# Performance work log

Hardware: AMD Instinct MI355X
Metric: run time of the kernel (lower is better)

## Reference

```python
import jax, jax.numpy as jnp
import numpy as np

EPS = 1e-12  # matches torch F.normalize eps

def _l2norm(v, axis):
    n = jnp.linalg.norm(v, axis=axis, keepdims=True)
    return v / jnp.maximum(n, EPS)

def setup_inputs() -> dict:
    key = jax.random.key(0)
    k1, k2 = jax.random.split(key)
    x = jax.random.normal(k1, (16, 512, 64, 64), dtype=jnp.float32)
    mem = jax.random.normal(k2, (1024, 512), dtype=jnp.float32)
    memory = _l2norm(mem, axis=1)  # buffer initialized normalized, as in __init__
    return {"x": x, "memory": memory}

def reference(x, memory):
    B, C, H, W = x.shape
    feat = x.transpose(0, 2, 3, 1).reshape(-1, C)          # [N, C], N=B*H*W
    feat_norm = _l2norm(feat, axis=1)                       # [N, C]
    mem_norm = _l2norm(memory, axis=1)                      # [K, C]
    sim = feat_norm @ mem_norm.T                            # [N, K] cosine sims
    attn = jax.nn.softmax(sim, axis=1)                      # [N, K]
    recon = attn @ mem_norm                                 # [N, C]
    recon = recon.reshape(B, H, W, C).transpose(0, 3, 1, 2) # [B, C, H, W]
    match_map = attn.max(axis=1).reshape(B, H, W)           # [B, H, W]
    return recon, match_map
```

## Files before the change

kernel.cpp:

```cpp
#include <hip/hip_runtime.h>

#define C_DIM 512
#define K_MEM 1024

typedef __attribute__((ext_vector_type(8))) short short8;
typedef __attribute__((ext_vector_type(4))) float f32x4;
typedef __attribute__((ext_vector_type(16))) float f32x16;
typedef __attribute__((ext_vector_type(4))) unsigned int u32x4;

#define LGKM0()  asm volatile("s_waitcnt lgkmcnt(0)" ::: "memory")
#define VM0()    asm volatile("s_waitcnt vmcnt(0)" ::: "memory")
#define BAR()    { asm volatile("" ::: "memory"); __builtin_amdgcn_s_barrier(); asm volatile("" ::: "memory"); }

#define GLOAD16(dst, addr, imm) \
    asm volatile("global_load_dwordx4 %0, %1, off offset:%c2" \
                 : "=v"(dst) : "v"(addr), "n"(imm))
#define WAITV(N) do { asm volatile("s_waitcnt vmcnt(%c0)" :: "n"(N) : "memory"); \
                      __builtin_amdgcn_sched_barrier(0); } while (0)

__device__ __forceinline__ unsigned short f2bf(float f) {
    unsigned int u = __builtin_bit_cast(unsigned int, f);
    unsigned int r = (u + 0x7fffu + ((u >> 16) & 1u)) >> 16;
    return (unsigned short)r;
}

__device__ __forceinline__ f32x4 mfma16(short8 a, short8 b, f32x4 c) {
    return __builtin_amdgcn_mfma_f32_16x16x32_bf16(a, b, c, 0, 0, 0);
}
__device__ __forceinline__ f32x16 mfma32(short8 a, short8 b, f32x16 c) {
    return __builtin_amdgcn_mfma_f32_32x32x16_bf16(a, b, c, 0, 0, 0);
}

__device__ __forceinline__ void gl_lds16(const void* g, void* l) {
    __builtin_amdgcn_global_load_lds(
        (const __attribute__((address_space(1))) unsigned int*)g,
        (__attribute__((address_space(3))) unsigned int*)l, 16, 0, 0);
}

__global__ __launch_bounds__(256)
void prep_norm(const float* __restrict__ mem, unsigned short* __restrict__ Mn) {
    int k = blockIdx.x, t = threadIdx.x;
    const float* row = mem + (size_t)k * C_DIM;
    float2 v = *reinterpret_cast<const float2*>(row + 2 * t);
    float ss = v.x * v.x + v.y * v.y;
#pragma unroll
    for (int off = 32; off >= 1; off >>= 1) ss += __shfl_xor(ss, off);
    __shared__ float wp[4];
    if ((t & 63) == 0) wp[t >> 6] = ss;
    __syncthreads();
    float tot = wp[0] + wp[1] + wp[2] + wp[3];
    float rn = 1.0f / fmaxf(sqrtf(tot), 1e-12f);
    unsigned int pk = (unsigned int)f2bf(v.x * rn) | ((unsigned int)f2bf(v.y * rn) << 16);
    *reinterpret_cast<unsigned int*>(Mn + (size_t)k * C_DIM + 2 * t) = pk;
}

__global__ __launch_bounds__(256)
void prep_transpose(const unsigned short* __restrict__ Mn, unsigned short* __restrict__ MnT) {
    __shared__ unsigned short tl[64][72];
    int t = threadIdx.x;
    int bk = blockIdx.x & 15, bc = blockIdx.x >> 4;
    int k0 = bk * 64, c0 = bc * 64;
    {
        int kr = t >> 2, gc = (t & 3) * 16;
        const u32x4* src = reinterpret_cast<const u32x4*>(Mn + (size_t)(k0 + kr) * C_DIM + c0 + gc);
        u32x4 a = src[0], b = src[1];
        *reinterpret_cast<u32x4*>(&tl[kr][gc]) = a;
        *reinterpret_cast<u32x4*>(&tl[kr][gc + 8]) = b;
    }
    __syncthreads();
    {
        int cr = t >> 2, gk = (t & 3) * 16;
        unsigned int ow[8];
#pragma unroll
        for (int j = 0; j < 8; ++j)
            ow[j] = (unsigned int)tl[gk + 2 * j][cr] | ((unsigned int)tl[gk + 2 * j + 1][cr] << 16);
        unsigned int* dst = reinterpret_cast<unsigned int*>(MnT + (size_t)(c0 + cr) * K_MEM + k0 + gk);
#pragma unroll
        for (int j = 0; j < 8; ++j) dst[j] = ow[j];
    }
}

__global__ __launch_bounds__(512)
void normx_kernel(const float* __restrict__ x, unsigned short* __restrict__ Fn) {
    __shared__ alignas(16) char FnB[65536];
    __shared__ float normpart[64][9];
    __shared__ float rnormS[64];
    const int t = threadIdx.x, bid = blockIdx.x;
    const int b = bid >> 6, h = bid & 63;
    const int lane = t & 63, wv = t >> 6;
    const int w = lane, cg = wv;
    const float* xp = x + (size_t)b * 2097152 + (size_t)(cg * 64) * 4096 + (size_t)h * 64 + w;
    float xv[64];
#pragma unroll
    for (int i = 0; i < 64; ++i) xv[i] = xp[(size_t)i * 4096];
    float ss = 0.f;
#pragma unroll
    for (int i = 0; i < 64; ++i) ss += xv[i] * xv[i];
    normpart[w][cg] = ss;
    __syncthreads();
    if (t < 64) {
        float s = 0.f;
#pragma unroll
        for (int j = 0; j < 8; ++j) s += normpart[t][j];
        rnormS[t] = 1.0f / fmaxf(sqrtf(s), 1e-12f);
    }
    __syncthreads();
    float rn = rnormS[w];
    char* fnrow = FnB + w * 1024;
#pragma unroll
    for (int j = 0; j < 8; ++j) {
        u32x4 pk4;
#pragma unroll
        for (int p = 0; p < 4; ++p) {
            float v0 = xv[j * 8 + 2 * p] * rn;
            float v1 = xv[j * 8 + 2 * p + 1] * rn;
            pk4[p] = (unsigned int)f2bf(v0) | ((unsigned int)f2bf(v1) << 16);
        }
        int gs = (cg * 8 + j) ^ (w & 31);
        *(u32x4*)(fnrow + (gs << 4)) = pk4;
    }
    __syncthreads();
    const int r = t >> 3;
    char* orow = (char*)(Fn + (size_t)(bid * 64 + r) * C_DIM);
#pragma unroll
    for (int p = 0; p < 8; ++p) {
        int gl = p * 8 + (t & 7);
        u32x4 v = *(const u32x4*)(FnB + r * 1024 + ((gl ^ (r & 31)) << 4));
        *(u32x4*)(orow + gl * 16) = v;
    }
}

__device__ __forceinline__ void stage_tile(const char* g0, size_t rowBytes, int col0,
                                           char* lds0, int wv, int lane) {
#pragma unroll
    for (int j = 0; j < 4; ++j) {
        const int chunk = wv * 4 + j;
        const int r = chunk * 8 + (lane >> 3);
        const int gs = (lane & 7) ^ (r & 7);
        const char* src = g0 + (size_t)r * rowBytes + col0 + gs * 16;
        gl_lds16(src, lds0 + chunk * 1024);
    }
}

#define FRAG(base, r, gk) (*(const short8*)((base) + (r) * 128 + ((((gk)) ^ ((r) & 7)) << 4)))

__global__ __launch_bounds__(256, 3)
void gemm1_kernel(const unsigned short* __restrict__ Fn, const unsigned short* __restrict__ Mn,
                  unsigned short* __restrict__ P, float* __restrict__ Zp, float* __restrict__ Mp) {
    __shared__ alignas(16) char LDSU[34816];
    __shared__ float zS[128][2], zM[128][2];
    char* As = LDSU;
    char* Bs = LDSU + 16384;

    const int wg = (blockIdx.x & 7) * 512 + (blockIdx.x >> 3);
    const int mt = wg >> 3, nt = wg & 7;
    const int m0 = mt * 128, n0 = nt * 128;
    const int t = threadIdx.x, lane = t & 63, wv = t >> 6;
    const int wm = wv >> 1, wn = wv & 1;
    const int l15 = lane & 15, l4 = lane >> 4;

    const char* Ag = (const char*)Fn + (size_t)m0 * 1024;
    const char* Bg = (const char*)Mn + (size_t)n0 * 1024;

    f32x4 acc[4][4];
#pragma unroll
    for (int i = 0; i < 4; ++i)
#pragma unroll
        for (int j = 0; j < 4; ++j) acc[i][j] = (f32x4){0.f, 0.f, 0.f, 0.f};

#pragma unroll 1
    for (int kt = 0; kt < 8; ++kt) {
        stage_tile(Ag, 1024, kt * 128, As, wv, lane);
        stage_tile(Bg, 1024, kt * 128, Bs, wv, lane);
        VM0(); BAR();
#pragma unroll
        for (int ks = 0; ks < 2; ++ks) {
            short8 af[4], bfr[4];
#pragma unroll
            for (int i = 0; i < 4; ++i) {
                af[i]  = FRAG(As, wm * 64 + i * 16 + l15, ks * 4 + l4);
                bfr[i] = FRAG(Bs, wn * 64 + i * 16 + l15, ks * 4 + l4);
            }
#pragma unroll
            for (int mf = 0; mf < 4; ++mf)
#pragma unroll
                for (int nf = 0; nf < 4; ++nf)
                    acc[mf][nf] = mfma16(af[mf], bfr[nf], acc[mf][nf]);
        }
        LGKM0(); BAR();
    }

    float zsum[4][4], zmax[4][4];
#pragma unroll
    for (int mf = 0; mf < 4; ++mf)
#pragma unroll
        for (int r = 0; r < 4; ++r) { zsum[mf][r] = 0.f; zmax[mf][r] = 0.f; }
#pragma unroll
    for (int mf = 0; mf < 4; ++mf)
#pragma unroll
        for (int nf = 0; nf < 4; ++nf)
#pragma unroll
            for (int r = 0; r < 4; ++r) {
                float e = __expf(acc[mf][nf][r]);
                acc[mf][nf][r] = e;
                zsum[mf][r] += e;
                zmax[mf][r] = fmaxf(zmax[mf][r], e);
            }
#pragma unroll
    for (int off = 1; off < 16; off <<= 1)
#pragma unroll
        for (int mf = 0; mf < 4; ++mf)
#pragma unroll
            for (int r = 0; r < 4; ++r) {
                zsum[mf][r] += __shfl_xor(zsum[mf][r], off);
                zmax[mf][r] = fmaxf(zmax[mf][r], __shfl_xor(zmax[mf][r], off));
            }
    if (l15 == 0) {
#pragma unroll
        for (int mf = 0; mf < 4; ++mf)
#pragma unroll
            for (int r = 0; r < 4; ++r) {
                int row = wm * 64 + mf * 16 + l4 * 4 + r;
                zS[row][wn] = zsum[mf][r];
                zM[row][wn] = zmax[mf][r];
            }
    }
    char* Pscr = LDSU;
#pragma unroll
    for (int mf = 0; mf < 4; ++mf)
#pragma unroll
        for (int nf = 0; nf < 4; ++nf)
#pragma unroll
            for (int r = 0; r < 4; ++r) {
                int row = wm * 64 + mf * 16 + l4 * 4 + r;
                int col = wn * 64 + nf * 16 + l15;
                *(unsigned short*)(Pscr + row * 272 + col * 2) = f2bf(acc[mf][nf][r]);
            }
    LGKM0(); BAR();
    if (t < 128) {
        float zq = zS[t][0] + zS[t][1];
        float mq = fmaxf(zM[t][0], zM[t][1]);
        Zp[(size_t)(m0 + t) * 8 + nt] = zq;
        Mp[(size_t)(m0 + t) * 8 + nt] = mq;
    }
#pragma unroll
    for (int p = 0; p < 8; ++p) {
        int r = (t >> 4) + p * 16;
        u32x4 v = *(const u32x4*)(Pscr + r * 272 + (t & 15) * 16);
        *(u32x4*)((char*)P + (size_t)(m0 + r) * 2048 + n0 * 2 + (t & 15) * 16) = v;
    }
}

__global__ __launch_bounds__(256)
void stats_kernel(const float* __restrict__ Zp, const float* __restrict__ Mp,
                  float* __restrict__ Zinv, float* __restrict__ match) {
    int i = blockIdx.x * 256 + threadIdx.x;
    f32x4 a = *(const f32x4*)(Zp + (size_t)i * 8);
    f32x4 b = *(const f32x4*)(Zp + (size_t)i * 8 + 4);
    float s = (a[0] + a[1] + a[2] + a[3]) + (b[0] + b[1] + b[2] + b[3]);
    f32x4 c = *(const f32x4*)(Mp + (size_t)i * 8);
    f32x4 d = *(const f32x4*)(Mp + (size_t)i * 8 + 4);
    float m = fmaxf(fmaxf(fmaxf(c[0], c[1]), fmaxf(c[2], c[3])),
                    fmaxf(fmaxf(d[0], d[1]), fmaxf(d[2], d[3])));
    float zi = 1.0f / s;
    Zinv[i] = zi;
    match[i] = m * zi;
}

__global__ __launch_bounds__(256, 3)
void gemm2_kernel(const unsigned short* __restrict__ P, const unsigned short* __restrict__ MnT,
                  const float* __restrict__ Zinv, float* __restrict__ recon) {
    __shared__ alignas(16) char As[16384];
    __shared__ alignas(16) char Bs[16384];
    __shared__ float zinvS[128];

    const int wg = (blockIdx.x & 7) * 256 + (blockIdx.x >> 3);
    const int mt = wg >> 2, nt = wg & 3;
    const int m0 = mt * 128, n0 = nt * 128;
    const int t = threadIdx.x, lane = t & 63, wv = t >> 6;
    const int wm = wv >> 1, wn = wv & 1;
    const int l15 = lane & 15, l4 = lane >> 4;

    if (t < 128) zinvS[t] = Zinv[m0 + t];

    const char* Ag = (const char*)P + (size_t)m0 * 2048;
    const char* Bg = (const char*)MnT + (size_t)n0 * 2048;

    f32x4 acc[4][4];
#pragma unroll
    for (int i = 0; i < 4; ++i)
#pragma unroll
        for (int j = 0; j < 4; ++j) acc[i][j] = (f32x4){0.f, 0.f, 0.f, 0.f};

#pragma unroll 1
    for (int kt = 0; kt < 16; ++kt) {
        stage_tile(Ag, 2048, kt * 128, As, wv, lane);
        stage_tile(Bg, 2048, kt * 128, Bs, wv, lane);
        VM0(); BAR();
#pragma unroll
        for (int ks = 0; ks < 2; ++ks) {
            short8 af[4], bfr[4];
#pragma unroll
            for (int i = 0; i < 4; ++i) {
                af[i]  = FRAG(As, wm * 64 + i * 16 + l15, ks * 4 + l4);
                bfr[i] = FRAG(Bs, wn * 64 + i * 16 + l15, ks * 4 + l4);
            }
#pragma unroll
            for (int mf = 0; mf < 4; ++mf)
#pragma unroll
                for (int nf = 0; nf < 4; ++nf)
                    acc[mf][nf] = mfma16(af[mf], bfr[nf], acc[mf][nf]);
        }
        LGKM0(); BAR();
    }

    const int b = m0 >> 12;
    const int inb0 = m0 & 4095;
#pragma unroll
    for (int mf = 0; mf < 4; ++mf) {
        f32x4 zv = *(const f32x4*)(&zinvS[wm * 64 + mf * 16 + l4 * 4]);
#pragma unroll
        for (int nf = 0; nf < 4; ++nf) {
            f32x4 v = acc[mf][nf];
            v[0] *= zv[0]; v[1] *= zv[1]; v[2] *= zv[2]; v[3] *= zv[3];
            int c = n0 + wn * 64 + nf * 16 + l15;
            int inb = inb0 + wm * 64 + mf * 16 + l4 * 4;
            *(f32x4*)(recon + (size_t)b * 2097152 + (size_t)c * 4096 + inb) = v;
        }
    }
}

__global__ __launch_bounds__(512)
__attribute__((amdgpu_waves_per_eu(2, 2)))
void fused_attn(const float* __restrict__ x,
                const unsigned short* __restrict__ Mn,
                const unsigned short* __restrict__ MnT,
                float* __restrict__ recon,
                float* __restrict__ match) {
    __shared__ alignas(16) char FnB[65536];
    __shared__ alignas(16) char PldsB[2 * 32768];
    __shared__ float Zinv[64], rnormS[64];

    const int t = threadIdx.x;
    const int bid = blockIdx.x;
    const int b = bid >> 6, h = bid & 63;
    const int lane = t & 63, wv = t >> 6;
    const int l31 = lane & 31, l5 = lane >> 5;
    const int ko = wv;
    const int cb = wv * 64;

    {
        float* normpart = (float*)PldsB;
        const int w = lane, cg = wv;
        const float* xp = x + (size_t)b * 2097152 + (size_t)(cg * 64) * 4096 + (size_t)h * 64 + w;
        float xv[64];
#pragma unroll
        for (int i = 0; i < 64; ++i) xv[i] = xp[(size_t)i * 4096];
        float ss = 0.f;
#pragma unroll
        for (int i = 0; i < 64; ++i) ss += xv[i] * xv[i];
        normpart[w * 9 + cg] = ss;
        __syncthreads();
        if (t < 64) {
            float s = 0.f;
#pragma unroll
            for (int j = 0; j < 8; ++j) s += normpart[t * 9 + j];
            rnormS[t] = 1.0f / fmaxf(sqrtf(s), 1e-12f);
        }
        __syncthreads();
        float rn = rnormS[w];
        char* fnrow = FnB + w * 1024;
#pragma unroll
        for (int j = 0; j < 8; ++j) {
            u32x4 pk4;
#pragma unroll
            for (int p = 0; p < 4; ++p) {
                float v0 = xv[j * 8 + 2 * p] * rn;
                float v1 = xv[j * 8 + 2 * p + 1] * rn;
                pk4[p] = (unsigned int)f2bf(v0) | ((unsigned int)f2bf(v1) << 16);
            }
            int gs = (cg * 8 + j) ^ (w & 31);
            *(u32x4*)(fnrow + (gs << 4)) = pk4;
        }
    }
    __syncthreads();

    f32x16 acc3[2][2];
#pragma unroll
    for (int i = 0; i < 2; ++i)
#pragma unroll
        for (int j = 0; j < 2; ++j)
#pragma unroll
            for (int r = 0; r < 16; ++r) acc3[i][j][r] = 0.f;

    float regZ[2] = {0.f, 0.f};
    float regM[2] = {-3.0e38f, -3.0e38f};
    const char* fnR0 = FnB + l31 * 1024;
    const char* fnR1 = FnB + (32 + l31) * 1024;

#pragma unroll 1
    for (int kt = 0; kt < 4; ++kt) {
        const char* aG = (const char*)Mn + ((size_t)(kt * 256 + ko * 32 + l31) << 10) + (l5 << 4);
        u32x4 afb[2][4];
        GLOAD16(afb[0][0], aG, 0);
        GLOAD16(afb[0][1], aG, 32);
        GLOAD16(afb[0][2], aG, 64);
        GLOAD16(afb[0][3], aG, 96);
        f32x16 acc1[2];
#pragma unroll
        for (int j = 0; j < 2; ++j)
#pragma unroll
            for (int r = 0; r < 16; ++r) acc1[j][r] = 0.f;
#pragma unroll
        for (int g = 0; g < 8; ++g) {
            if (g < 7) {
#pragma unroll
                for (int s = 0; s < 4; ++s)
                    GLOAD16(afb[(g + 1) & 1][s], aG, ((g + 1) * 4 + s) * 32);
                WAITV(4);
            } else {
                WAITV(0);
            }
#pragma unroll
            for (int s = 0; s < 4; ++s) {
                const int st = g * 4 + s;
                const int gsw = (((st << 1) | l5) ^ l31) << 4;
                short8 b0 = *(const short8*)(fnR0 + gsw);
                short8 b1 = *(const short8*)(fnR1 + gsw);
                short8 av = __builtin_bit_cast(short8, afb[g & 1][s]);
                acc1[0] = mfma32(av, b0, acc1[0]);
                acc1[1] = mfma32(av, b1, acc1[1]);
            }
        }
        const char* aG2a = (const char*)MnT + ((size_t)(cb + l31) << 11) + ((size_t)kt << 9) + (l5 << 4);
        const char* aG2b = aG2a + 65536;
        u32x4 a2b[2][4];
        GLOAD16(a2b[0][0], aG2a, 0);
        GLOAD16(a2b[0][1], aG2b, 0);
        GLOAD16(a2b[0][2], aG2a, 32);
        GLOAD16(a2b[0][3], aG2b, 32);
        unsigned int P32[2][8];
#pragma unroll
        for (int nt = 0; nt < 2; ++nt) {
            float s0 = 0.f, m0 = -3.0e38f;
#pragma unroll
            for (int j = 0; j < 8; ++j) {
                float a0 = acc1[nt][2 * j], a1 = acc1[nt][2 * j + 1];
                m0 = fmaxf(m0, fmaxf(a0, a1));
                float e0 = __expf(a0), e1 = __expf(a1);
                P32[nt][j] = (unsigned int)f2bf(e0) | ((unsigned int)f2bf(e1) << 16);
                s0 += e0 + e1;
            }
            s0 += __shfl_xor(s0, 32);
            m0 = fmaxf(m0, __shfl_xor(m0, 32));
            regZ[nt] += s0;
            regM[nt] = fmaxf(regM[nt], m0);
        }
        char* Pb = PldsB + (kt & 1) * 32768;
#pragma unroll
        for (int nt = 0; nt < 2; ++nt) {
            const int n = nt * 32 + l31;
            char* prow = Pb + n * 512;
#pragma unroll
            for (int jp = 0; jp < 4; ++jp) {
                const int gk = ko * 4 + jp;
                uint2 v;
                v.x = P32[nt][2 * jp];
                v.y = P32[nt][2 * jp + 1];
                *(uint2*)(prow + ((gk ^ (n & 31)) << 4) + 8 * l5) = v;
            }
        }
        LGKM0(); BAR();
#pragma unroll
        for (int g = 0; g < 8; ++g) {
            if (g < 7) {
#pragma unroll
                for (int u = 0; u < 2; ++u) {
                    GLOAD16(a2b[(g + 1) & 1][u * 2 + 0], aG2a, ((g + 1) * 2 + u) * 32);
                    GLOAD16(a2b[(g + 1) & 1][u * 2 + 1], aG2b, ((g + 1) * 2 + u) * 32);
                }
                WAITV(4);
            } else {
                WAITV(0);
            }
#pragma unroll
            for (int u = 0; u < 2; ++u) {
                const int ks = g * 2 + u;
                const int gsw = (((ks << 1) | l5) ^ l31) << 4;
                short8 bp0 = *(const short8*)(Pb + l31 * 512 + gsw);
                short8 bp1 = *(const short8*)(Pb + (32 + l31) * 512 + gsw);
                short8 a0 = __builtin_bit_cast(short8, a2b[g & 1][u * 2 + 0]);
                short8 a1 = __builtin_bit_cast(short8, a2b[g & 1][u * 2 + 1]);
                acc3[0][0] = mfma32(a0, bp0, acc3[0][0]);
                acc3[0][1] = mfma32(a0, bp1, acc3[0][1]);
                acc3[1][0] = mfma32(a1, bp0, acc3[1][0]);
                acc3[1][1] = mfma32(a1, bp1, acc3[1][1]);
            }
        }
    }
    {
        float* pS = (float*)FnB;
        float* pM = (float*)(FnB + 2048);
        if (l5 == 0) {
            pS[ko * 64 + l31] = regZ[0];
            pS[ko * 64 + 32 + l31] = regZ[1];
            pM[ko * 64 + l31] = regM[0];
            pM[ko * 64 + 32 + l31] = regM[1];
        }
        LGKM0(); BAR();
        if (t < 64) {
            float s = 0.f, m = -3.0e38f;
#pragma unroll
            for (int k8 = 0; k8 < 8; ++k8) {
                s += pS[k8 * 64 + t];
                m = fmaxf(m, pM[k8 * 64 + t]);
            }
            float zi = 1.0f / s;
            Zinv[t] = zi;
            match[(size_t)bid * 64 + t] = __expf(m) * zi;
        }
        LGKM0(); BAR();
    }
    const float zi0 = Zinv[l31], zi1 = Zinv[32 + l31];
    float* rbase = recon + (size_t)b * 2097152 + (size_t)h * 64;
#pragma unroll
    for (int ct = 0; ct < 2; ++ct) {
#pragma unroll
        for (int r = 0; r < 16; ++r) {
            const int c = cb + ct * 32 + (r & 3) + 8 * (r >> 2) + 4 * l5;
            float* rp = rbase + (size_t)c * 4096;
            rp[l31] = acc3[ct][0][r] * zi0;
            rp[32 + l31] = acc3[ct][1][r] * zi1;
        }
    }
}

extern "C" void kernel_launch(void* const* d_in, const int* in_sizes, int n_in,
                              void* d_out, int out_size, void* d_ws, size_t ws_size,
                              hipStream_t stream) {
    (void)in_sizes; (void)n_in; (void)out_size;
    if (ws_size < (size_t)2 * 1024 * 1024) return;

    const float* x = (const float*)d_in[0];
    const float* mem = (const float*)d_in[1];
    float* recon = (float*)d_out;
    float* match = recon + (size_t)16 * 512 * 64 * 64;
    char* ws = (char*)d_ws;
    unsigned short* Mn = (unsigned short*)ws;
    unsigned short* MnT = (unsigned short*)(ws + 1048576);

    prep_norm<<<dim3(K_MEM), dim3(256), 0, stream>>>(mem, Mn);
    prep_transpose<<<dim3(128), dim3(256), 0, stream>>>(Mn, MnT);

    const size_t NEED = 207880192ull;
    if (ws_size >= NEED) {
        unsigned short* Fn = (unsigned short*)(ws + 2097152);
        unsigned short* P  = (unsigned short*)(ws + 69206016);
        float* Zp   = (float*)(ws + 203423744);
        float* Mp   = (float*)(ws + 205520896);
        float* Zi   = (float*)(ws + 207618048);
        normx_kernel<<<dim3(1024), dim3(512), 0, stream>>>(x, Fn);
        gemm1_kernel<<<dim3(4096), dim3(256), 0, stream>>>(Fn, Mn, P, Zp, Mp);
        stats_kernel<<<dim3(256), dim3(256), 0, stream>>>(Zp, Mp, Zi, match);
        gemm2_kernel<<<dim3(2048), dim3(256), 0, stream>>>(P, MnT, Zi, recon);
    } else {
        fused_attn<<<dim3(1024), dim3(512), 0, stream>>>(x, Mn, MnT, recon, match);
    }
}
```

Before: 250.1 us.

## Use 256x256 double-buffered GEMM tiles with prefetch and MFMA priority

```diff
diff --git a/kernel.cpp b/kernel.cpp
--- a/kernel.cpp
+++ b/kernel.cpp
@@ -11,6 +11,7 @@
 #define LGKM0()  asm volatile("s_waitcnt lgkmcnt(0)" ::: "memory")
 #define VM0()    asm volatile("s_waitcnt vmcnt(0)" ::: "memory")
 #define BAR()    { asm volatile("" ::: "memory"); __builtin_amdgcn_s_barrier(); asm volatile("" ::: "memory"); }
+#define SCHED0() __builtin_amdgcn_sched_barrier(0)
 
 #define GLOAD16(dst, addr, imm) \
     asm volatile("global_load_dwordx4 %0, %1, off offset:%c2" \
@@ -130,124 +131,144 @@
     }
 }
 
-__device__ __forceinline__ void stage_tile(const char* g0, size_t rowBytes, int col0,
-                                           char* lds0, int wv, int lane) {
-#pragma unroll
-    for (int j = 0; j < 4; ++j) {
-        const int chunk = wv * 4 + j;
-        const int r = chunk * 8 + (lane >> 3);
-        const int gs = (lane & 7) ^ (r & 7);
-        const char* src = g0 + (size_t)r * rowBytes + col0 + gs * 16;
-        gl_lds16(src, lds0 + chunk * 1024);
-    }
-}
-
+__device__ __forceinline__ void stage64(const char* g0, int rowBytes, int kcol,
+                                        char* ldsChunk, int j, int wv, int lane) {
+    const int rloc = wv * 8 + (lane >> 3);
+    const int rglob = j * 64 + rloc;
+    const int gs = (lane & 7) ^ (rloc & 7);
+    gl_lds16(g0 + (size_t)rglob * rowBytes + kcol + gs * 16, ldsChunk + wv * 1024);
+}
 #define FRAG(base, r, gk) (*(const short8*)((base) + (r) * 128 + ((((gk)) ^ ((r) & 7)) << 4)))
 
-__global__ __launch_bounds__(256, 3)
+#define GEMM_KLOOP(NKT, ABYT, BBYT)                                                   \
+    {                                                                                  \
+        for (int j = 0; j < 4; ++j) stage64(Ag, ABYT, 0, LDSU + j * 8192, j, wv, lane); \
+        for (int j = 0; j < 4; ++j) stage64(Bg, BBYT, 0, LDSU + 32768 + j * 8192, j, wv, lane); \
+        VM0(); BAR();                                                                   \
+    }                                                                                  \
+    _Pragma("unroll 1")                                                                \
+    for (int kt = 0; kt < (NKT); ++kt) {                                               \
+        char* Asp = LDSU + (kt & 1) * 65536;                                           \
+        char* Bsp = Asp + 32768;                                                       \
+        char* Asn = LDSU + ((kt + 1) & 1) * 65536;                                     \
+        char* Bsn = Asn + 32768;                                                       \
+        const int kcoln = (kt + 1) * 128;                                              \
+        _Pragma("unroll")                                                              \
+        for (int s = 0; s < 2; ++s) {                                                  \
+            short8 af[4], bfv[4];                                                      \
+            if (s == 0 && kt + 1 < (NKT)) {                                            \
+                _Pragma("unroll")                                                      \
+                for (int j = 0; j < 4; ++j)                                            \
+                    stage64(Ag, ABYT, kcoln, Asn + j * 8192, j, wv, lane);             \
+            }                                                                          \
+            _Pragma("unroll")                                                          \
+            for (int i = 0; i < 4; ++i) bfv[i] = FRAG(Bsp, wn * 64 + i * 16 + l15, s * 4 + l4); \
+            _Pragma("unroll")                                                          \
+            for (int i = 0; i < 4; ++i) af[i] = FRAG(Asp, wm * 128 + i * 16 + l15, s * 4 + l4); \
+            SCHED0();                                                                  \
+            __builtin_amdgcn_s_setprio(1);                                             \
+            _Pragma("unroll")                                                          \
+            for (int mf = 0; mf < 4; ++mf)                                             \
+                _Pragma("unroll")                                                      \
+                for (int nf = 0; nf < 4; ++nf)                                         \
+                    acc[mf][nf] = mfma16(af[mf], bfv[nf], acc[mf][nf]);                \
+            __builtin_amdgcn_s_setprio(0);                                             \
+            SCHED0();                                                                  \
+            if (s == 0 && kt + 1 < (NKT)) {                                            \
+                _Pragma("unroll")                                                      \
+                for (int j = 0; j < 4; ++j)                                            \
+                    stage64(Bg, BBYT, kcoln, Bsn + j * 8192, j, wv, lane);             \
+            }                                                                          \
+            _Pragma("unroll")                                                          \
+            for (int i = 0; i < 4; ++i) af[i] = FRAG(Asp, wm * 128 + (4 + i) * 16 + l15, s * 4 + l4); \
+            SCHED0();                                                                  \
+            __builtin_amdgcn_s_setprio(1);                                             \
+            _Pragma("unroll")                                                          \
+            for (int mf = 0; mf < 4; ++mf)                                             \
+                _Pragma("unroll")                                                      \
+                for (int nf = 0; nf < 4; ++nf)                                         \
+                    acc[4 + mf][nf] = mfma16(af[mf], bfv[nf], acc[4 + mf][nf]);        \
+            __builtin_amdgcn_s_setprio(0);                                             \
+            SCHED0();                                                                  \
+        }                                                                              \
+        if (kt + 1 < (NKT)) VM0();                                                     \
+        BAR();                                                                         \
+    }
+
+__global__ __launch_bounds__(512)
+__attribute__((amdgpu_waves_per_eu(2, 2)))
 void gemm1_kernel(const unsigned short* __restrict__ Fn, const unsigned short* __restrict__ Mn,
                   unsigned short* __restrict__ P, float* __restrict__ Zp, float* __restrict__ Mp) {
-    __shared__ alignas(16) char LDSU[34816];
-    __shared__ float zS[128][2], zM[128][2];
-    char* As = LDSU;
-    char* Bs = LDSU + 16384;
-
-    const int wg = (blockIdx.x & 7) * 512 + (blockIdx.x >> 3);
-    const int mt = wg >> 3, nt = wg & 7;
-    const int m0 = mt * 128, n0 = nt * 128;
+    __shared__ alignas(16) char LDSU[135168];
+    __shared__ float zS[256][4], zM[256][4];
+
+    const int wg = (blockIdx.x & 7) * 128 + (blockIdx.x >> 3);
+    const int mt = wg >> 2, ntile = wg & 3;
+    const int m0 = mt * 256, n0 = ntile * 256;
     const int t = threadIdx.x, lane = t & 63, wv = t >> 6;
-    const int wm = wv >> 1, wn = wv & 1;
+    const int wm = wv >> 2, wn = wv & 3;
     const int l15 = lane & 15, l4 = lane >> 4;
 
     const char* Ag = (const char*)Fn + (size_t)m0 * 1024;
     const char* Bg = (const char*)Mn + (size_t)n0 * 1024;
 
-    f32x4 acc[4][4];
-#pragma unroll
-    for (int i = 0; i < 4; ++i)
+    f32x4 acc[8][4];
+#pragma unroll
+    for (int i = 0; i < 8; ++i)
 #pragma unroll
         for (int j = 0; j < 4; ++j) acc[i][j] = (f32x4){0.f, 0.f, 0.f, 0.f};
 
-#pragma unroll 1
-    for (int kt = 0; kt < 8; ++kt) {
-        stage_tile(Ag, 1024, kt * 128, As, wv, lane);
-        stage_tile(Bg, 1024, kt * 128, Bs, wv, lane);
-        VM0(); BAR();
-#pragma unroll
-        for (int ks = 0; ks < 2; ++ks) {
-            short8 af[4], bfr[4];
-#pragma unroll
-            for (int i = 0; i < 4; ++i) {
-                af[i]  = FRAG(As, wm * 64 + i * 16 + l15, ks * 4 + l4);
-                bfr[i] = FRAG(Bs, wn * 64 + i * 16 + l15, ks * 4 + l4);
-            }
-#pragma unroll
-            for (int mf = 0; mf < 4; ++mf)
-#pragma unroll
-                for (int nf = 0; nf < 4; ++nf)
-                    acc[mf][nf] = mfma16(af[mf], bfr[nf], acc[mf][nf]);
-        }
-        LGKM0(); BAR();
-    }
-
-    float zsum[4][4], zmax[4][4];
-#pragma unroll
-    for (int mf = 0; mf < 4; ++mf)
-#pragma unroll
-        for (int r = 0; r < 4; ++r) { zsum[mf][r] = 0.f; zmax[mf][r] = 0.f; }
-#pragma unroll
-    for (int mf = 0; mf < 4; ++mf)
-#pragma unroll
-        for (int nf = 0; nf < 4; ++nf)
+    GEMM_KLOOP(8, 1024, 1024)
+
+    char* Pscr = LDSU;
+#pragma unroll
+    for (int mf = 0; mf < 8; ++mf) {
+        float zs[4] = {0.f, 0.f, 0.f, 0.f};
+        float zm[4] = {0.f, 0.f, 0.f, 0.f};
+#pragma unroll
+        for (int nf = 0; nf < 4; ++nf) {
+            const int col = wn * 64 + nf * 16 + l15;
 #pragma unroll
             for (int r = 0; r < 4; ++r) {
                 float e = __expf(acc[mf][nf][r]);
-                acc[mf][nf][r] = e;
-                zsum[mf][r] += e;
-                zmax[mf][r] = fmaxf(zmax[mf][r], e);
-            }
-#pragma unroll
-    for (int off = 1; off < 16; off <<= 1)
-#pragma unroll
-        for (int mf = 0; mf < 4; ++mf)
+                zs[r] += e;
+                zm[r] = fmaxf(zm[r], e);
+                const int row = wm * 128 + mf * 16 + l4 * 4 + r;
+                *(unsigned short*)(Pscr + row * 528 + col * 2) = f2bf(e);
+            }
+        }
+#pragma unroll
+        for (int off = 1; off < 16; off <<= 1)
 #pragma unroll
             for (int r = 0; r < 4; ++r) {
-                zsum[mf][r] += __shfl_xor(zsum[mf][r], off);
-                zmax[mf][r] = fmaxf(zmax[mf][r], __shfl_xor(zmax[mf][r], off));
-            }
-    if (l15 == 0) {
-#pragma unroll
-        for (int mf = 0; mf < 4; ++mf)
+                zs[r] += __shfl_xor(zs[r], off);
+                zm[r] = fmaxf(zm[r], __shfl_xor(zm[r], off));
+            }
+        if (l15 == 0) {
 #pragma unroll
             for (int r = 0; r < 4; ++r) {
-                int row = wm * 64 + mf * 16 + l4 * 4 + r;
-                zS[row][wn] = zsum[mf][r];
-                zM[row][wn] = zmax[mf][r];
-            }
-    }
-    char* Pscr = LDSU;
-#pragma unroll
-    for (int mf = 0; mf < 4; ++mf)
-#pragma unroll
-        for (int nf = 0; nf < 4; ++nf)
-#pragma unroll
-            for (int r = 0; r < 4; ++r) {
-                int row = wm * 64 + mf * 16 + l4 * 4 + r;
-                int col = wn * 64 + nf * 16 + l15;
-                *(unsigned short*)(Pscr + row * 272 + col * 2) = f2bf(acc[mf][nf][r]);
-            }
+                const int row = wm * 128 + mf * 16 + l4 * 4 + r;
+                zS[row][wn] = zs[r];
+                zM[row][wn] = zm[r];
+            }
+        }
+    }
     LGKM0(); BAR();
-    if (t < 128) {
-        float zq = zS[t][0] + zS[t][1];
-        float mq = fmaxf(zM[t][0], zM[t][1]);
-        Zp[(size_t)(m0 + t) * 8 + nt] = zq;
-        Mp[(size_t)(m0 + t) * 8 + nt] = mq;
+    if (t < 256) {
+        float zq = zS[t][0] + zS[t][1] + zS[t][2] + zS[t][3];
+        float mq = fmaxf(fmaxf(zM[t][0], zM[t][1]), fmaxf(zM[t][2], zM[t][3]));
+        Zp[(size_t)(m0 + t) * 4 + ntile] = zq;
+        Mp[(size_t)(m0 + t) * 4 + ntile] = mq;
     }
 #pragma unroll
     for (int p = 0; p < 8; ++p) {
-        int r = (t >> 4) + p * 16;
-        u32x4 v = *(const u32x4*)(Pscr + r * 272 + (t & 15) * 16);
-        *(u32x4*)((char*)P + (size_t)(m0 + r) * 2048 + n0 * 2 + (t & 15) * 16) = v;
+        const int r = p * 32 + (t >> 4);
+        const char* src = Pscr + r * 528 + (t & 15) * 32;
+        char* dst = (char*)P + (size_t)(m0 + r) * 2048 + n0 * 2 + (t & 15) * 32;
+        u32x4 v0 = *(const u32x4*)src;
+        u32x4 v1 = *(const u32x4*)(src + 16);
+        *(u32x4*)dst = v0;
+        *(u32x4*)(dst + 16) = v1;
     }
 }
 
@@ -255,76 +276,53 @@
 void stats_kernel(const float* __restrict__ Zp, const float* __restrict__ Mp,
                   float* __restrict__ Zinv, float* __restrict__ match) {
     int i = blockIdx.x * 256 + threadIdx.x;
-    f32x4 a = *(const f32x4*)(Zp + (size_t)i * 8);
-    f32x4 b = *(const f32x4*)(Zp + (size_t)i * 8 + 4);
-    float s = (a[0] + a[1] + a[2] + a[3]) + (b[0] + b[1] + b[2] + b[3]);
-    f32x4 c = *(const f32x4*)(Mp + (size_t)i * 8);
-    f32x4 d = *(const f32x4*)(Mp + (size_t)i * 8 + 4);
-    float m = fmaxf(fmaxf(fmaxf(c[0], c[1]), fmaxf(c[2], c[3])),
-                    fmaxf(fmaxf(d[0], d[1]), fmaxf(d[2], d[3])));
+    f32x4 a = *(const f32x4*)(Zp + (size_t)i * 4);
+    f32x4 c = *(const f32x4*)(Mp + (size_t)i * 4);
+    float s = a[0] + a[1] + a[2] + a[3];
+    float m = fmaxf(fmaxf(c[0], c[1]), fmaxf(c[2], c[3]));
     float zi = 1.0f / s;
     Zinv[i] = zi;
     match[i] = m * zi;
 }
 
-__global__ __launch_bounds__(256, 3)
+__global__ __launch_bounds__(512)
+__attribute__((amdgpu_waves_per_eu(2, 2)))
 void gemm2_kernel(const unsigned short* __restrict__ P, const unsigned short* __restrict__ MnT,
                   const float* __restrict__ Zinv, float* __restrict__ recon) {
-    __shared__ alignas(16) char As[16384];
-    __shared__ alignas(16) char Bs[16384];
-    __shared__ float zinvS[128];
-
-    const int wg = (blockIdx.x & 7) * 256 + (blockIdx.x >> 3);
-    const int mt = wg >> 2, nt = wg & 3;
-    const int m0 = mt * 128, n0 = nt * 128;
+    __shared__ alignas(16) char LDSU[131072];
+    __shared__ float zinvS[256];
+
+    const int wg = (blockIdx.x & 7) * 64 + (blockIdx.x >> 3);
+    const int mt = wg >> 1, ntile = wg & 1;
+    const int m0 = mt * 256, n0 = ntile * 256;
     const int t = threadIdx.x, lane = t & 63, wv = t >> 6;
-    const int wm = wv >> 1, wn = wv & 1;
+    const int wm = wv >> 2, wn = wv & 3;
     const int l15 = lane & 15, l4 = lane >> 4;
 
-    if (t < 128) zinvS[t] = Zinv[m0 + t];
+    if (t < 256) zinvS[t] = Zinv[m0 + t];
 
     const char* Ag = (const char*)P + (size_t)m0 * 2048;
     const char* Bg = (const char*)MnT + (size_t)n0 * 2048;
 
-    f32x4 acc[4][4];
-#pragma unroll
-    for (int i = 0; i < 4; ++i)
+    f32x4 acc[8][4];
+#pragma unroll
+    for (int i = 0; i < 8; ++i)
 #pragma unroll
         for (int j = 0; j < 4; ++j) acc[i][j] = (f32x4){0.f, 0.f, 0.f, 0.f};
 
-#pragma unroll 1
-    for (int kt = 0; kt < 16; ++kt) {
-        stage_tile(Ag, 2048, kt * 128, As, wv, lane);
-        stage_tile(Bg, 2048, kt * 128, Bs, wv, lane);
-        VM0(); BAR();
-#pragma unroll
-        for (int ks = 0; ks < 2; ++ks) {
-            short8 af[4], bfr[4];
-#pragma unroll
-            for (int i = 0; i < 4; ++i) {
-                af[i]  = FRAG(As, wm * 64 + i * 16 + l15, ks * 4 + l4);
-                bfr[i] = FRAG(Bs, wn * 64 + i * 16 + l15, ks * 4 + l4);
-            }
-#pragma unroll
-            for (int mf = 0; mf < 4; ++mf)
-#pragma unroll
-                for (int nf = 0; nf < 4; ++nf)
-                    acc[mf][nf] = mfma16(af[mf], bfr[nf], acc[mf][nf]);
-        }
-        LGKM0(); BAR();
-    }
+    GEMM_KLOOP(16, 2048, 2048)
 
     const int b = m0 >> 12;
     const int inb0 = m0 & 4095;
 #pragma unroll
-    for (int mf = 0; mf < 4; ++mf) {
-        f32x4 zv = *(const f32x4*)(&zinvS[wm * 64 + mf * 16 + l4 * 4]);
+    for (int mf = 0; mf < 8; ++mf) {
+        f32x4 zv = *(const f32x4*)(&zinvS[wm * 128 + mf * 16 + l4 * 4]);
 #pragma unroll
         for (int nf = 0; nf < 4; ++nf) {
             f32x4 v = acc[mf][nf];
             v[0] *= zv[0]; v[1] *= zv[1]; v[2] *= zv[2]; v[3] *= zv[3];
-            int c = n0 + wn * 64 + nf * 16 + l15;
-            int inb = inb0 + wm * 64 + mf * 16 + l4 * 4;
+            const int c = n0 + wn * 64 + nf * 16 + l15;
+            const int inb = inb0 + wm * 128 + mf * 16 + l4 * 4;
             *(f32x4*)(recon + (size_t)b * 2097152 + (size_t)c * 4096 + inb) = v;
         }
     }
@@ -552,17 +550,17 @@
     prep_norm<<<dim3(K_MEM), dim3(256), 0, stream>>>(mem, Mn);
     prep_transpose<<<dim3(128), dim3(256), 0, stream>>>(Mn, MnT);
 
-    const size_t NEED = 207880192ull;
+    const size_t NEED = 205783040ull;
     if (ws_size >= NEED) {
         unsigned short* Fn = (unsigned short*)(ws + 2097152);
         unsigned short* P  = (unsigned short*)(ws + 69206016);
-        float* Zp   = (float*)(ws + 203423744);
-        float* Mp   = (float*)(ws + 205520896);
-        float* Zi   = (float*)(ws + 207618048);
+        float* Zp = (float*)(ws + 203423744);
+        float* Mp = (float*)(ws + 204472320);
+        float* Zi = (float*)(ws + 205520896);
         normx_kernel<<<dim3(1024), dim3(512), 0, stream>>>(x, Fn);
-        gemm1_kernel<<<dim3(4096), dim3(256), 0, stream>>>(Fn, Mn, P, Zp, Mp);
+        gemm1_kernel<<<dim3(1024), dim3(512), 0, stream>>>(Fn, Mn, P, Zp, Mp);
         stats_kernel<<<dim3(256), dim3(256), 0, stream>>>(Zp, Mp, Zi, match);
-        gemm2_kernel<<<dim3(2048), dim3(256), 0, stream>>>(P, MnT, Zi, recon);
+        gemm2_kernel<<<dim3(512), dim3(512), 0, stream>>>(P, MnT, Zi, recon);
     } else {
         fused_attn<<<dim3(1024), dim3(512), 0, stream>>>(x, Mn, MnT, recon, match);
     }
```

After: 276.7 us. 10.6% more time.

## Widen GEMM tiles to 128x256 with 8 waves and fold stats into gemm2

Applied to the files above, without the earlier changes.

```diff
diff --git a/kernel.cpp b/kernel.cpp
--- a/kernel.cpp
+++ b/kernel.cpp
@@ -130,35 +130,59 @@
     }
 }
 
-__device__ __forceinline__ void stage_tile(const char* g0, size_t rowBytes, int col0,
-                                           char* lds0, int wv, int lane) {
-#pragma unroll
-    for (int j = 0; j < 4; ++j) {
-        const int chunk = wv * 4 + j;
-        const int r = chunk * 8 + (lane >> 3);
+template <int R>
+__device__ __forceinline__ void stageT(const char* g0, size_t rowBytes, int col0,
+                                       char* lds0, int wv, int lane) {
+    const int per = R / 8;
+#pragma unroll
+    for (int j = 0; j < per / 8; ++j) {
+        const int r = wv * per + j * 8 + (lane >> 3);
         const int gs = (lane & 7) ^ (r & 7);
-        const char* src = g0 + (size_t)r * rowBytes + col0 + gs * 16;
-        gl_lds16(src, lds0 + chunk * 1024);
+        gl_lds16(g0 + (size_t)r * rowBytes + col0 + gs * 16,
+                 lds0 + (wv * (per / 8) + j) * 1024);
     }
 }
 
 #define FRAG(base, r, gk) (*(const short8*)((base) + (r) * 128 + ((((gk)) ^ ((r) & 7)) << 4)))
 
-__global__ __launch_bounds__(256, 3)
+#define GEMM_KLOOP(NKT, ABYT, BBYT)                                                     \
+    _Pragma("unroll 1")                                                                  \
+    for (int kt = 0; kt < (NKT); ++kt) {                                                 \
+        stageT<128>(Ag, ABYT, kt * 128, As, wv, lane);                                   \
+        stageT<256>(Bg, BBYT, kt * 128, Bs, wv, lane);                                   \
+        VM0(); BAR();                                                                    \
+        _Pragma("unroll")                                                                \
+        for (int ks = 0; ks < 2; ++ks) {                                                 \
+            short8 af[4], bfr[4];                                                        \
+            _Pragma("unroll")                                                            \
+            for (int i = 0; i < 4; ++i) {                                                \
+                af[i]  = FRAG(As, wm * 64 + i * 16 + l15, ks * 4 + l4);                  \
+                bfr[i] = FRAG(Bs, wn * 64 + i * 16 + l15, ks * 4 + l4);                  \
+            }                                                                            \
+            _Pragma("unroll")                                                            \
+            for (int mf = 0; mf < 4; ++mf)                                               \
+                _Pragma("unroll")                                                        \
+                for (int nf = 0; nf < 4; ++nf)                                           \
+                    acc[mf][nf] = mfma16(af[mf], bfr[nf], acc[mf][nf]);                  \
+        }                                                                                \
+        LGKM0(); BAR();                                                                  \
+    }
+
+__global__ __launch_bounds__(512, 4)
 void gemm1_kernel(const unsigned short* __restrict__ Fn, const unsigned short* __restrict__ Mn,
                   unsigned short* __restrict__ P, float* __restrict__ Zp, float* __restrict__ Mp) {
-    __shared__ alignas(16) char LDSU[34816];
-    __shared__ float zS[128][2], zM[128][2];
+    __shared__ alignas(16) char LDSU[67584];
+    __shared__ float zS[128][4], zM[128][4];
+
+    const int wg = (blockIdx.x & 7) * 256 + (blockIdx.x >> 3);
+    const int mt = wg >> 2, ntile = wg & 3;
+    const int m0 = mt * 128, n0 = ntile * 256;
+    const int t = threadIdx.x, lane = t & 63, wv = t >> 6;
+    const int wm = wv >> 2, wn = wv & 3;
+    const int l15 = lane & 15, l4 = lane >> 4;
+
     char* As = LDSU;
     char* Bs = LDSU + 16384;
-
-    const int wg = (blockIdx.x & 7) * 512 + (blockIdx.x >> 3);
-    const int mt = wg >> 3, nt = wg & 7;
-    const int m0 = mt * 128, n0 = nt * 128;
-    const int t = threadIdx.x, lane = t & 63, wv = t >> 6;
-    const int wm = wv >> 1, wn = wv & 1;
-    const int l15 = lane & 15, l4 = lane >> 4;
-
     const char* Ag = (const char*)Fn + (size_t)m0 * 1024;
     const char* Bg = (const char*)Mn + (size_t)n0 * 1024;
 
@@ -168,28 +192,9 @@
 #pragma unroll
         for (int j = 0; j < 4; ++j) acc[i][j] = (f32x4){0.f, 0.f, 0.f, 0.f};
 
-#pragma unroll 1
-    for (int kt = 0; kt < 8; ++kt) {
-        stage_tile(Ag, 1024, kt * 128, As, wv, lane);
-        stage_tile(Bg, 1024, kt * 128, Bs, wv, lane);
-        VM0(); BAR();
-#pragma unroll
-        for (int ks = 0; ks < 2; ++ks) {
-            short8 af[4], bfr[4];
-#pragma unroll
-            for (int i = 0; i < 4; ++i) {
-                af[i]  = FRAG(As, wm * 64 + i * 16 + l15, ks * 4 + l4);
-                bfr[i] = FRAG(Bs, wn * 64 + i * 16 + l15, ks * 4 + l4);
-            }
-#pragma unroll
-            for (int mf = 0; mf < 4; ++mf)
-#pragma unroll
-                for (int nf = 0; nf < 4; ++nf)
-                    acc[mf][nf] = mfma16(af[mf], bfr[nf], acc[mf][nf]);
-        }
-        LGKM0(); BAR();
-    }
-
+    GEMM_KLOOP(8, 1024, 1024)
+
+    char* Pscr = LDSU;
     float zsum[4][4], zmax[4][4];
 #pragma unroll
     for (int mf = 0; mf < 4; ++mf)
@@ -220,69 +225,64 @@
         for (int mf = 0; mf < 4; ++mf)
 #pragma unroll
             for (int r = 0; r < 4; ++r) {
-                int row = wm * 64 + mf * 16 + l4 * 4 + r;
+                const int row = wm * 64 + mf * 16 + l4 * 4 + r;
                 zS[row][wn] = zsum[mf][r];
                 zM[row][wn] = zmax[mf][r];
             }
     }
-    char* Pscr = LDSU;
 #pragma unroll
     for (int mf = 0; mf < 4; ++mf)
 #pragma unroll
         for (int nf = 0; nf < 4; ++nf)
 #pragma unroll
             for (int r = 0; r < 4; ++r) {
-                int row = wm * 64 + mf * 16 + l4 * 4 + r;
-                int col = wn * 64 + nf * 16 + l15;
-                *(unsigned short*)(Pscr + row * 272 + col * 2) = f2bf(acc[mf][nf][r]);
+                const int row = wm * 64 + mf * 16 + l4 * 4 + r;
+                const int col = wn * 64 + nf * 16 + l15;
+                *(unsigned short*)(Pscr + row * 528 + col * 2) = f2bf(acc[mf][nf][r]);
             }
     LGKM0(); BAR();
     if (t < 128) {
-        float zq = zS[t][0] + zS[t][1];
-        float mq = fmaxf(zM[t][0], zM[t][1]);
-        Zp[(size_t)(m0 + t) * 8 + nt] = zq;
-        Mp[(size_t)(m0 + t) * 8 + nt] = mq;
+        float zq = zS[t][0] + zS[t][1] + zS[t][2] + zS[t][3];
+        float mq = fmaxf(fmaxf(zM[t][0], zM[t][1]), fmaxf(zM[t][2], zM[t][3]));
+        Zp[(size_t)(m0 + t) * 4 + ntile] = zq;
+        Mp[(size_t)(m0 + t) * 4 + ntile] = mq;
     }
 #pragma unroll
     for (int p = 0; p < 8; ++p) {
-        int r = (t >> 4) + p * 16;
-        u32x4 v = *(const u32x4*)(Pscr + r * 272 + (t & 15) * 16);
-        *(u32x4*)((char*)P + (size_t)(m0 + r) * 2048 + n0 * 2 + (t & 15) * 16) = v;
-    }
-}
-
-__global__ __launch_bounds__(256)
-void stats_kernel(const float* __restrict__ Zp, const float* __restrict__ Mp,
-                  float* __restrict__ Zinv, float* __restrict__ match) {
-    int i = blockIdx.x * 256 + threadIdx.x;
-    f32x4 a = *(const f32x4*)(Zp + (size_t)i * 8);
-    f32x4 b = *(const f32x4*)(Zp + (size_t)i * 8 + 4);
-    float s = (a[0] + a[1] + a[2] + a[3]) + (b[0] + b[1] + b[2] + b[3]);
-    f32x4 c = *(const f32x4*)(Mp + (size_t)i * 8);
-    f32x4 d = *(const f32x4*)(Mp + (size_t)i * 8 + 4);
-    float m = fmaxf(fmaxf(fmaxf(c[0], c[1]), fmaxf(c[2], c[3])),
-                    fmaxf(fmaxf(d[0], d[1]), fmaxf(d[2], d[3])));
-    float zi = 1.0f / s;
-    Zinv[i] = zi;
-    match[i] = m * zi;
-}
-
-__global__ __launch_bounds__(256, 3)
+        const int r = p * 16 + (t >> 5);
+        u32x4 v = *(const u32x4*)(Pscr + r * 528 + (t & 31) * 16);
+        *(u32x4*)((char*)P + (size_t)(m0 + r) * 2048 + n0 * 2 + (t & 31) * 16) = v;
+    }
+}
+
+__global__ __launch_bounds__(512, 4)
 void gemm2_kernel(const unsigned short* __restrict__ P, const unsigned short* __restrict__ MnT,
-                  const float* __restrict__ Zinv, float* __restrict__ recon) {
-    __shared__ alignas(16) char As[16384];
-    __shared__ alignas(16) char Bs[16384];
+                  const float* __restrict__ Zp, const float* __restrict__ Mp,
+                  float* __restrict__ recon, float* __restrict__ match) {
+    __shared__ alignas(16) char LDSU[49152];
     __shared__ float zinvS[128];
 
-    const int wg = (blockIdx.x & 7) * 256 + (blockIdx.x >> 3);
-    const int mt = wg >> 2, nt = wg & 3;
-    const int m0 = mt * 128, n0 = nt * 128;
+    const int wg = (blockIdx.x & 7) * 128 + (blockIdx.x >> 3);
+    const int mt = wg >> 1, ntile = wg & 1;
+    const int m0 = mt * 128, n0 = ntile * 256;
     const int t = threadIdx.x, lane = t & 63, wv = t >> 6;
-    const int wm = wv >> 1, wn = wv & 1;
+    const int wm = wv >> 2, wn = wv & 3;
     const int l15 = lane & 15, l4 = lane >> 4;
 
-    if (t < 128) zinvS[t] = Zinv[m0 + t];
-
+    if (t < 128) {
+        f32x4 zp = *(const f32x4*)(Zp + (size_t)(m0 + t) * 4);
+        float s = zp[0] + zp[1] + zp[2] + zp[3];
+        float zi = 1.0f / s;
+        zinvS[t] = zi;
+        if (ntile == 0) {
+            f32x4 mp = *(const f32x4*)(Mp + (size_t)(m0 + t) * 4);
+            float m = fmaxf(fmaxf(mp[0], mp[1]), fmaxf(mp[2], mp[3]));
+            match[m0 + t] = m * zi;
+        }
+    }
+
+    char* As = LDSU;
+    char* Bs = LDSU + 16384;
     const char* Ag = (const char*)P + (size_t)m0 * 2048;
     const char* Bg = (const char*)MnT + (size_t)n0 * 2048;
 
@@ -292,27 +292,7 @@
 #pragma unroll
         for (int j = 0; j < 4; ++j) acc[i][j] = (f32x4){0.f, 0.f, 0.f, 0.f};
 
-#pragma unroll 1
-    for (int kt = 0; kt < 16; ++kt) {
-        stage_tile(Ag, 2048, kt * 128, As, wv, lane);
-        stage_tile(Bg, 2048, kt * 128, Bs, wv, lane);
-        VM0(); BAR();
-#pragma unroll
-        for (int ks = 0; ks < 2; ++ks) {
-            short8 af[4], bfr[4];
-#pragma unroll
-            for (int i = 0; i < 4; ++i) {
-                af[i]  = FRAG(As, wm * 64 + i * 16 + l15, ks * 4 + l4);
-                bfr[i] = FRAG(Bs, wn * 64 + i * 16 + l15, ks * 4 + l4);
-            }
-#pragma unroll
-            for (int mf = 0; mf < 4; ++mf)
-#pragma unroll
-                for (int nf = 0; nf < 4; ++nf)
-                    acc[mf][nf] = mfma16(af[mf], bfr[nf], acc[mf][nf]);
-        }
-        LGKM0(); BAR();
-    }
+    GEMM_KLOOP(16, 2048, 2048)
 
     const int b = m0 >> 12;
     const int inb0 = m0 & 4095;
@@ -323,8 +303,8 @@
         for (int nf = 0; nf < 4; ++nf) {
             f32x4 v = acc[mf][nf];
             v[0] *= zv[0]; v[1] *= zv[1]; v[2] *= zv[2]; v[3] *= zv[3];
-            int c = n0 + wn * 64 + nf * 16 + l15;
-            int inb = inb0 + wm * 64 + mf * 16 + l4 * 4;
+            const int c = n0 + wn * 64 + nf * 16 + l15;
+            const int inb = inb0 + wm * 64 + mf * 16 + l4 * 4;
             *(f32x4*)(recon + (size_t)b * 2097152 + (size_t)c * 4096 + inb) = v;
         }
     }
@@ -552,17 +532,15 @@
     prep_norm<<<dim3(K_MEM), dim3(256), 0, stream>>>(mem, Mn);
     prep_transpose<<<dim3(128), dim3(256), 0, stream>>>(Mn, MnT);
 
-    const size_t NEED = 207880192ull;
+    const size_t NEED = 205520896ull;
     if (ws_size >= NEED) {
         unsigned short* Fn = (unsigned short*)(ws + 2097152);
         unsigned short* P  = (unsigned short*)(ws + 69206016);
-        float* Zp   = (float*)(ws + 203423744);
-        float* Mp   = (float*)(ws + 205520896);
-        float* Zi   = (float*)(ws + 207618048);
+        float* Zp = (float*)(ws + 203423744);
+        float* Mp = (float*)(ws + 204472320);
         normx_kernel<<<dim3(1024), dim3(512), 0, stream>>>(x, Fn);
-        gemm1_kernel<<<dim3(4096), dim3(256), 0, stream>>>(Fn, Mn, P, Zp, Mp);
-        stats_kernel<<<dim3(256), dim3(256), 0, stream>>>(Zp, Mp, Zi, match);
-        gemm2_kernel<<<dim3(2048), dim3(256), 0, stream>>>(P, MnT, Zi, recon);
+        gemm1_kernel<<<dim3(2048), dim3(512), 0, stream>>>(Fn, Mn, P, Zp, Mp);
+        gemm2_kernel<<<dim3(1024), dim3(512), 0, stream>>>(P, MnT, Zp, Mp, recon, match);
     } else {
         fused_attn<<<dim3(1024), dim3(512), 0, stream>>>(x, Mn, MnT, recon, match);
     }
```

After: 266.2 us. 6.4% more time.
